# Performance work log

Measured on AMD Instinct MI355X. Metric: run time of the kernel, lower is better.

Reference implementation:

```python
import jax, jax.numpy as jnp
import numpy as np

N = 50000              # total nodes
E = 800000             # random edges (self loops added inside reference, as PyG GATConv does)
FD = 3                 # feature_dim_node
C = 64                 # hidden_channels (= out after heads=1 concat)
OUT = 64               # out_channels of conv2
FC = 512               # fc_hidden_dim
NODES_PER_GRAPH = 5000
NUM_GRAPHS = N // NODES_PER_GRAPH
NEG_SLOPE = 0.2        # PyG GATConv default negative_slope


def _gat(x, W, a_s, a_d, b, src, dst):
    """Single-head PyG GATConv: gather -> leaky_relu -> segment softmax over dst -> scatter-sum."""
    n = x.shape[0]
    h = x @ W                       # [N, C]
    e_s = h @ a_s                   # [N] alpha contribution of source nodes
    e_d = h @ a_d                   # [N] alpha contribution of dest nodes
    e = e_s[src] + e_d[dst]         # [E+N] per-edge logits
    e = jnp.where(e > 0, e, NEG_SLOPE * e)  # leaky_relu
    m = jax.ops.segment_max(e, dst, num_segments=n)
    p = jnp.exp(e - m[dst])
    s = jax.ops.segment_sum(p, dst, num_segments=n)
    alpha = p / s[dst]              # segment softmax over incoming edges of each dst
    out = jax.ops.segment_sum(alpha[:, None] * h[src], dst, num_segments=n)
    return out + b


def setup_inputs() -> dict:
    key = jax.random.key(0)
    ks = jax.random.split(key, 20)
    p = lambda k, shape: (jax.random.normal(k, shape, jnp.float32) * 0.1)
    inp = {
        "x": jax.random.normal(ks[0], (N, FD), jnp.float32),
        "edge_index": jax.random.randint(ks[1], (2, E), 0, N, jnp.int64),
        # conv1: FD -> C
        "W1": p(ks[2], (FD, C)), "as1": p(ks[3], (C,)), "ad1": p(ks[4], (C,)), "b1": p(ks[5], (C,)),
        # 2 hidden convs: C -> C (num_layers - 2 = 2)
        "Wh": p(ks[6], (2, C, C)), "ash": p(ks[7], (2, C)), "adh": p(ks[8], (2, C)), "bh": p(ks[9], (2, C)),
        # conv2: C -> OUT
        "W2": p(ks[10], (C, OUT)), "as2": p(ks[11], (OUT,)), "ad2": p(ks[12], (OUT,)), "b2": p(ks[13], (OUT,)),
        # value head MLP
        "Wv1": p(ks[14], (OUT, FC)), "bv1": p(ks[15], (FC,)),
        "Wv2": p(ks[16], (FC, 1)), "bv2": p(ks[17], (1,)),
    }
    return inp


def reference(x, edge_index, W1, as1, ad1, b1, Wh, ash, adh, bh,
              W2, as2, ad2, b2, Wv1, bv1, Wv2, bv2):
    loops = jnp.arange(N, dtype=edge_index.dtype)
    src = jnp.concatenate([edge_index[0], loops])   # add self loops (PyG default)
    dst = jnp.concatenate([edge_index[1], loops])

    h = jax.nn.relu(_gat(x, W1, as1, ad1, b1, src, dst))
    for i in range(2):  # fixed small layer loop
        h = jax.nn.relu(_gat(h, Wh[i], ash[i], adh[i], bh[i], src, dst))
    h = _gat(h, W2, as2, ad2, b2, src, dst)          # [N, OUT] node embeddings (no relu)

    batch = jnp.arange(N) // NODES_PER_GRAPH          # create_batch_tensor
    pooled = jax.ops.segment_sum(h, batch, num_segments=NUM_GRAPHS) / NODES_PER_GRAPH
    value = jax.nn.relu(pooled @ Wv1 + bv1) @ Wv2 + bv2   # [NUM_GRAPHS, 1]
    return h, pooled, value
```

## Files before the change

### kernel.cpp

```cpp
#include <hip/hip_runtime.h>
#include <hip/hip_fp16.h>
#include <math.h>

#define NN 50000
#define EE 800000
#define TOT_EDGES (EE + NN)
#define FD 3
#define C 64
#define FC 512
#define NODES_PER_GRAPH 5000
#define NUM_GRAPHS 10
#define POOL_CHUNKS 40
#define POOL_NODES_PER_CHUNK 125
#define NEG_SLOPE 0.2f

#define SCAN_BLK 1024
#define SCAN_GRID ((NN + SCAN_BLK - 1) / SCAN_BLK)

#define HC_BLOCKS 1024

#define NPART 8
#define PART_NODES ((NN + NPART - 1) / NPART)
#define CSR_EPT 8
#define CSR_CHUNK (256 * CSR_EPT)
#define CSR_CHUNKS ((TOT_EDGES + CSR_CHUNK - 1) / CSR_CHUNK)


__global__ void k_init_counts(int* counts) {
    int i = blockIdx.x * blockDim.x + threadIdx.x;
    if (i < NN) counts[i] = 0;
}

__global__ void k_count_part(const int* __restrict__ dst, int* __restrict__ counts) {
    int part = blockIdx.x & (NPART - 1);
    int chunk = blockIdx.x >> 3;
    int lo = part * PART_NODES, hi = lo + PART_NODES;
    int base = chunk * CSR_CHUNK + threadIdx.x;
#pragma unroll
    for (int e = 0; e < CSR_EPT; ++e) {
        int i = base + e * 256;
        if (i < TOT_EDGES) {
            int d = (i < EE) ? dst[i] : (i - EE);
            if (d >= lo && d < hi) atomicAdd(&counts[d], 1);
        }
    }
}

__global__ void k_scan1(const int* __restrict__ counts, int* __restrict__ offsets,
                        int* __restrict__ blocksums) {
    int tid = threadIdx.x, blk = blockIdx.x;
    int i = blk * SCAN_BLK + tid;
    int v = (i < NN) ? counts[i] : 0;
    __shared__ int buf[SCAN_BLK];
    buf[tid] = v;
    __syncthreads();
    for (int off = 1; off < SCAN_BLK; off <<= 1) {
        int t = (tid >= off) ? buf[tid - off] : 0;
        __syncthreads();
        buf[tid] += t;
        __syncthreads();
    }
    if (i < NN) offsets[i] = buf[tid] - v;
    if (tid == SCAN_BLK - 1) blocksums[blk] = buf[tid];
}

__global__ void k_scan2(int* __restrict__ blocksums, int* __restrict__ offsets) {
    if (threadIdx.x == 0) {
        int run = 0;
        for (int b = 0; b < SCAN_GRID; ++b) {
            int v = blocksums[b];
            blocksums[b] = run;
            run += v;
        }
        offsets[NN] = run;
    }
}

__global__ void k_scan3(int* __restrict__ offsets, int* __restrict__ cursors,
                        const int* __restrict__ blocksums) {
    int tid = threadIdx.x, blk = blockIdx.x;
    int i = blk * SCAN_BLK + tid;
    if (i < NN) {
        int o = offsets[i] + blocksums[blk];
        offsets[i] = o;
        cursors[i] = o;
    }
}

__global__ void k_scatter_part(const int* __restrict__ src, const int* __restrict__ dst,
                               int* __restrict__ cursors, int* __restrict__ ssrc) {
    int part = blockIdx.x & (NPART - 1);
    int chunk = blockIdx.x >> 3;
    int lo = part * PART_NODES, hi = lo + PART_NODES;
    int base = chunk * CSR_CHUNK + threadIdx.x;
#pragma unroll
    for (int e = 0; e < CSR_EPT; ++e) {
        int i = base + e * 256;
        if (i < TOT_EDGES) {
            int d = (i < EE) ? dst[i] : (i - EE);
            if (d >= lo && d < hi) {
                int s = (i < EE) ? src[i] : d;
                int idx = atomicAdd(&cursors[d], 1);
                ssrc[idx] = s;
            }
        }
    }
}


template<int IN_DIM>
__global__ void k_hcompute_t(const float* __restrict__ x,
                             const float* __restrict__ W,
                             const float* __restrict__ a_s, const float* __restrict__ a_d,
                             __half* __restrict__ h, float* __restrict__ es,
                             float* __restrict__ ed, int nwaves_total) {
    int lane = threadIdx.x & 63;
    int wid = (blockIdx.x * blockDim.x + threadIdx.x) >> 6;

    float wcol[IN_DIM];
#pragma unroll
    for (int k = 0; k < IN_DIM; ++k) wcol[k] = W[k * 64 + lane];
    float asl = a_s[lane], adl = a_d[lane];

    for (int n = wid; n < NN; n += nwaves_total) {
        int nu = __builtin_amdgcn_readfirstlane(n);
        const float* xrow = x + (size_t)nu * IN_DIM;
        float acc = 0.f;
#pragma unroll
        for (int k = 0; k < IN_DIM; ++k) acc = fmaf(xrow[k], wcol[k], acc);
        h[(size_t)nu * 64 + lane] = __float2half(acc);
        float vs = acc * asl;
        float vd = acc * adl;
        for (int w = 32; w >= 1; w >>= 1) {
            vs += __shfl_xor(vs, w);
            vd += __shfl_xor(vd, w);
        }
        if (lane == 0) { es[nu] = vs; ed[nu] = vd; }
    }
}

__global__ void k_aggregate(const __half* __restrict__ h,
                            const float* __restrict__ es, const float* __restrict__ ed,
                            const int* __restrict__ offsets, const int* __restrict__ ssrc,
                            const float* __restrict__ bias,
                            float* __restrict__ out, int do_relu) {
    int gtid = blockIdx.x * blockDim.x + threadIdx.x;
    int n = gtid >> 6;
    int lane = threadIdx.x & 63;
    if (n >= NN) return;
    int beg = offsets[n], end = offsets[n + 1];
    float edn = ed[n];

    int grp = lane >> 3;
    int c   = lane & 7;
    float s = 0.f;
    float acc[8];
#pragma unroll
    for (int i = 0; i < 8; ++i) acc[i] = 0.f;

    for (int j0 = beg; j0 < end; j0 += 8) {
        int jg = j0 + grp;
        if (jg < end) {
            int sj = ssrc[jg];
            float e = es[sj] + edn;
            e = (e > 0.f) ? e : NEG_SLOPE * e;
            float p = __expf(e);
            s += p;
            float4 raw = *(const float4*)&h[(size_t)sj * 64 + c * 8];
            const __half2* hp = (const __half2*)&raw;
#pragma unroll
            for (int q = 0; q < 4; ++q) {
                float2 f = __half22float2(hp[q]);
                acc[2 * q]     = fmaf(p, f.x, acc[2 * q]);
                acc[2 * q + 1] = fmaf(p, f.y, acc[2 * q + 1]);
            }
        }
    }
#pragma unroll
    for (int w = 8; w <= 32; w <<= 1) {
        s += __shfl_xor(s, w);
#pragma unroll
        for (int i = 0; i < 8; ++i) acc[i] += __shfl_xor(acc[i], w);
    }
    if (grp == 0) {
        float inv_s = 1.0f / s;
        float v[8];
#pragma unroll
        for (int i = 0; i < 8; ++i) {
            v[i] = acc[i] * inv_s + bias[c * 8 + i];
            if (do_relu) v[i] = fmaxf(v[i], 0.f);
        }
        *(float4*)&out[(size_t)n * 64 + c * 8]     = make_float4(v[0], v[1], v[2], v[3]);
        *(float4*)&out[(size_t)n * 64 + c * 8 + 4] = make_float4(v[4], v[5], v[6], v[7]);
    }
}


__global__ void k_pool1(const float* __restrict__ h, float* __restrict__ partial) {
    int blk = blockIdx.x;
    int g = blk / POOL_CHUNKS, c = blk % POOL_CHUNKS;
    int wave = threadIdx.x >> 6, lane = threadIdx.x & 63;
    int base = g * NODES_PER_GRAPH + c * POOL_NODES_PER_CHUNK;
    float acc = 0.f;
    for (int i = wave; i < POOL_NODES_PER_CHUNK; i += 4)
        acc += h[(size_t)(base + i) * 64 + lane];
    __shared__ float buf[4][64];
    buf[wave][lane] = acc;
    __syncthreads();
    if (wave == 0)
        partial[blk * 64 + lane] = buf[0][lane] + buf[1][lane] + buf[2][lane] + buf[3][lane];
}

__global__ void k_pool2(const float* __restrict__ partial, float* __restrict__ pooled) {
    int g = blockIdx.x;
    int lane = threadIdx.x;
    float acc = 0.f;
    for (int c = 0; c < POOL_CHUNKS; ++c)
        acc += partial[(g * POOL_CHUNKS + c) * 64 + lane];
    pooled[g * 64 + lane] = acc * (1.0f / NODES_PER_GRAPH);
}

__global__ void k_value(const float* __restrict__ pooled,
                        const float* __restrict__ Wv1, const float* __restrict__ bv1,
                        const float* __restrict__ Wv2, const float* __restrict__ bv2,
                        float* __restrict__ value) {
    int g = blockIdx.x;
    int j = threadIdx.x;
    __shared__ float pl[64];
    if (j < 64) pl[j] = pooled[g * 64 + j];
    __syncthreads();
    float acc = bv1[j];
    for (int c = 0; c < 64; ++c) acc += pl[c] * Wv1[c * 512 + j];
    acc = fmaxf(acc, 0.f);
    float t = acc * Wv2[j];
    for (int w = 32; w >= 1; w >>= 1) t += __shfl_xor(t, w);
    __shared__ float red[8];
    int wave = j >> 6, lane = j & 63;
    if (lane == 0) red[wave] = t;
    __syncthreads();
    if (j == 0) {
        float v = 0.f;
        for (int w = 0; w < 8; ++w) v += red[w];
        value[g] = v + bv2[0];
    }
}


extern "C" void kernel_launch(void* const* d_in, const int* in_sizes, int n_in,
                              void* d_out, int out_size, void* d_ws, size_t ws_size,
                              hipStream_t stream) {
    const float* x   = (const float*)d_in[0];
    const int*   ei  = (const int*)d_in[1];
    const float* W1  = (const float*)d_in[2];
    const float* as1 = (const float*)d_in[3];
    const float* ad1 = (const float*)d_in[4];
    const float* b1  = (const float*)d_in[5];
    const float* Wh  = (const float*)d_in[6];
    const float* ash = (const float*)d_in[7];
    const float* adh = (const float*)d_in[8];
    const float* bh  = (const float*)d_in[9];
    const float* W2  = (const float*)d_in[10];
    const float* as2 = (const float*)d_in[11];
    const float* ad2 = (const float*)d_in[12];
    const float* b2  = (const float*)d_in[13];
    const float* Wv1 = (const float*)d_in[14];
    const float* bv1 = (const float*)d_in[15];
    const float* Wv2 = (const float*)d_in[16];
    const float* bv2 = (const float*)d_in[17];

    const int* e_src = ei;
    const int* e_dst = ei + EE;

    char* p = (char*)d_ws;
    auto carve = [&](size_t bytes) {
        char* r = p;
        p += (bytes + 255) & ~(size_t)255;
        return r;
    };
    int*    counts    = (int*)carve(NN * 4);
    int*    offsets   = (int*)carve((NN + 1) * 4);
    int*    cursors   = (int*)carve(NN * 4);
    int*    ssrc      = (int*)carve(TOT_EDGES * 4);
    int*    blocksums = (int*)carve(SCAN_GRID * 4);
    __half* bufH      = (__half*)carve((size_t)NN * 64 * 2);
    float*  bufB      = (float*)carve((size_t)NN * 64 * 4);
    float*  es        = (float*)carve(NN * 4);
    float*  ed        = (float*)carve(NN * 4);
    float*  partial   = (float*)carve((size_t)NUM_GRAPHS * POOL_CHUNKS * 64 * 4);

    float* out_h      = (float*)d_out;
    float* out_pooled = out_h + (size_t)NN * 64;
    float* out_value  = out_pooled + NUM_GRAPHS * 64;

    k_init_counts<<<(NN + 255) / 256, 256, 0, stream>>>(counts);
    k_count_part<<<NPART * CSR_CHUNKS, 256, 0, stream>>>(e_dst, counts);
    k_scan1<<<SCAN_GRID, SCAN_BLK, 0, stream>>>(counts, offsets, blocksums);
    k_scan2<<<1, 64, 0, stream>>>(blocksums, offsets);
    k_scan3<<<SCAN_GRID, SCAN_BLK, 0, stream>>>(offsets, cursors, blocksums);
    k_scatter_part<<<NPART * CSR_CHUNKS, 256, 0, stream>>>(e_src, e_dst, cursors, ssrc);

    const int HBLK = (NN + 3) / 4;
    const int HC_WAVES = HC_BLOCKS * 256 / 64;

    k_hcompute_t<FD><<<HC_BLOCKS, 256, 0, stream>>>(x, W1, as1, ad1, bufH, es, ed, HC_WAVES);
    k_aggregate<<<HBLK, 256, 0, stream>>>(bufH, es, ed, offsets, ssrc, b1, bufB, 1);

    for (int i = 0; i < 2; ++i) {
        k_hcompute_t<C><<<HC_BLOCKS, 256, 0, stream>>>(bufB, Wh + i * 64 * 64, ash + i * 64,
                                                       adh + i * 64, bufH, es, ed, HC_WAVES);
        k_aggregate<<<HBLK, 256, 0, stream>>>(bufH, es, ed, offsets, ssrc, bh + i * 64, bufB, 1);
    }

    k_hcompute_t<C><<<HC_BLOCKS, 256, 0, stream>>>(bufB, W2, as2, ad2, bufH, es, ed, HC_WAVES);
    k_aggregate<<<HBLK, 256, 0, stream>>>(bufH, es, ed, offsets, ssrc, b2, out_h, 0);

    k_pool1<<<NUM_GRAPHS * POOL_CHUNKS, 256, 0, stream>>>(out_h, partial);
    k_pool2<<<NUM_GRAPHS, 64, 0, stream>>>(partial, out_pooled);
    k_value<<<NUM_GRAPHS, 512, 0, stream>>>(out_pooled, Wv1, bv1, Wv2, bv2, out_value);
}
```

Measured before the change: 290.6 us.

## Fuse next-layer linear transform and attention logits into aggregation kernel

```diff
diff --git a/kernel.cpp b/kernel.cpp
--- a/kernel.cpp
+++ b/kernel.cpp
@@ -18,6 +18,7 @@
 #define SCAN_GRID ((NN + SCAN_BLK - 1) / SCAN_BLK)
 
 #define HC_BLOCKS 1024
+#define AGG_BLOCKS 1024
 
 #define NPART 8
 #define PART_NODES ((NN + NPART - 1) / NPART)
@@ -139,59 +140,95 @@
     }
 }
 
-__global__ void k_aggregate(const __half* __restrict__ h,
+template<int HAS_NEXT>
+__global__ void k_agg_fused(const __half* __restrict__ h,
                             const float* __restrict__ es, const float* __restrict__ ed,
                             const int* __restrict__ offsets, const int* __restrict__ ssrc,
                             const float* __restrict__ bias,
-                            float* __restrict__ out, int do_relu) {
-    int gtid = blockIdx.x * blockDim.x + threadIdx.x;
-    int n = gtid >> 6;
+                            const float* __restrict__ Wn,
+                            const float* __restrict__ asn, const float* __restrict__ adn,
+                            __half* __restrict__ hn, float* __restrict__ esn,
+                            float* __restrict__ edn_out,
+                            float* __restrict__ out_final,
+                            int nwaves_total) {
     int lane = threadIdx.x & 63;
-    if (n >= NN) return;
-    int beg = offsets[n], end = offsets[n + 1];
-    float edn = ed[n];
-
+    int wid = (blockIdx.x * blockDim.x + threadIdx.x) >> 6;
     int grp = lane >> 3;
     int c   = lane & 7;
-    float s = 0.f;
-    float acc[8];
-#pragma unroll
-    for (int i = 0; i < 8; ++i) acc[i] = 0.f;
-
-    for (int j0 = beg; j0 < end; j0 += 8) {
-        int jg = j0 + grp;
-        if (jg < end) {
-            int sj = ssrc[jg];
-            float e = es[sj] + edn;
-            e = (e > 0.f) ? e : NEG_SLOPE * e;
-            float p = __expf(e);
-            s += p;
-            float4 raw = *(const float4*)&h[(size_t)sj * 64 + c * 8];
-            const __half2* hp = (const __half2*)&raw;
-#pragma unroll
-            for (int q = 0; q < 4; ++q) {
-                float2 f = __half22float2(hp[q]);
-                acc[2 * q]     = fmaf(p, f.x, acc[2 * q]);
-                acc[2 * q + 1] = fmaf(p, f.y, acc[2 * q + 1]);
-            }
-        }
-    }
-#pragma unroll
-    for (int w = 8; w <= 32; w <<= 1) {
-        s += __shfl_xor(s, w);
-#pragma unroll
-        for (int i = 0; i < 8; ++i) acc[i] += __shfl_xor(acc[i], w);
-    }
-    if (grp == 0) {
+
+    float wn[HAS_NEXT ? 64 : 1];
+    float asl = 0.f, adl = 0.f;
+    if (HAS_NEXT) {
+#pragma unroll
+        for (int k = 0; k < 64; ++k) wn[k] = Wn[k * 64 + lane];
+        asl = asn[lane];
+        adl = adn[lane];
+    }
+    float4 blo = *(const float4*)&bias[c * 8];
+    float4 bhi = *(const float4*)&bias[c * 8 + 4];
+    float bb[8] = {blo.x, blo.y, blo.z, blo.w, bhi.x, bhi.y, bhi.z, bhi.w};
+
+    for (int n = wid; n < NN; n += nwaves_total) {
+        int beg = offsets[n], end = offsets[n + 1];
+        float ednv = ed[n];
+        float s = 0.f;
+        float acc[8];
+#pragma unroll
+        for (int i = 0; i < 8; ++i) acc[i] = 0.f;
+
+        for (int j0 = beg; j0 < end; j0 += 8) {
+            int jg = j0 + grp;
+            if (jg < end) {
+                int sj = ssrc[jg];
+                float e = es[sj] + ednv;
+                e = (e > 0.f) ? e : NEG_SLOPE * e;
+                float p = __expf(e);
+                s += p;
+                float4 raw = *(const float4*)&h[(size_t)sj * 64 + c * 8];
+                const __half2* hp = (const __half2*)&raw;
+#pragma unroll
+                for (int q = 0; q < 4; ++q) {
+                    float2 f = __half22float2(hp[q]);
+                    acc[2 * q]     = fmaf(p, f.x, acc[2 * q]);
+                    acc[2 * q + 1] = fmaf(p, f.y, acc[2 * q + 1]);
+                }
+            }
+        }
+#pragma unroll
+        for (int w = 8; w <= 32; w <<= 1) {
+            s += __shfl_xor(s, w);
+#pragma unroll
+            for (int i = 0; i < 8; ++i) acc[i] += __shfl_xor(acc[i], w);
+        }
         float inv_s = 1.0f / s;
         float v[8];
 #pragma unroll
         for (int i = 0; i < 8; ++i) {
-            v[i] = acc[i] * inv_s + bias[c * 8 + i];
-            if (do_relu) v[i] = fmaxf(v[i], 0.f);
-        }
-        *(float4*)&out[(size_t)n * 64 + c * 8]     = make_float4(v[0], v[1], v[2], v[3]);
-        *(float4*)&out[(size_t)n * 64 + c * 8 + 4] = make_float4(v[4], v[5], v[6], v[7]);
+            v[i] = acc[i] * inv_s + bb[i];
+            if (HAS_NEXT) v[i] = fmaxf(v[i], 0.f);
+        }
+
+        if (HAS_NEXT) {
+            float hv = 0.f;
+#pragma unroll
+            for (int k = 0; k < 64; ++k) {
+                float rowk = __shfl(v[k & 7], k >> 3);
+                hv = fmaf(rowk, wn[k], hv);
+            }
+            hn[(size_t)n * 64 + lane] = __float2half(hv);
+            float vs = hv * asl;
+            float vd = hv * adl;
+            for (int w = 32; w >= 1; w >>= 1) {
+                vs += __shfl_xor(vs, w);
+                vd += __shfl_xor(vd, w);
+            }
+            if (lane == 0) { esn[n] = vs; edn_out[n] = vd; }
+        } else {
+            if (grp == 0) {
+                *(float4*)&out_final[(size_t)n * 64 + c * 8]     = make_float4(v[0], v[1], v[2], v[3]);
+                *(float4*)&out_final[(size_t)n * 64 + c * 8 + 4] = make_float4(v[4], v[5], v[6], v[7]);
+            }
+        }
     }
 }
 
@@ -282,10 +319,12 @@
     int*    cursors   = (int*)carve(NN * 4);
     int*    ssrc      = (int*)carve(TOT_EDGES * 4);
     int*    blocksums = (int*)carve(SCAN_GRID * 4);
-    __half* bufH      = (__half*)carve((size_t)NN * 64 * 2);
-    float*  bufB      = (float*)carve((size_t)NN * 64 * 4);
-    float*  es        = (float*)carve(NN * 4);
-    float*  ed        = (float*)carve(NN * 4);
+    __half* bufHA     = (__half*)carve((size_t)NN * 64 * 2);
+    __half* bufHB     = (__half*)carve((size_t)NN * 64 * 2);
+    float*  esA       = (float*)carve(NN * 4);
+    float*  edA       = (float*)carve(NN * 4);
+    float*  esB       = (float*)carve(NN * 4);
+    float*  edB       = (float*)carve(NN * 4);
     float*  partial   = (float*)carve((size_t)NUM_GRAPHS * POOL_CHUNKS * 64 * 4);
 
     float* out_h      = (float*)d_out;
@@ -299,20 +338,23 @@
     k_scan3<<<SCAN_GRID, SCAN_BLK, 0, stream>>>(offsets, cursors, blocksums);
     k_scatter_part<<<NPART * CSR_CHUNKS, 256, 0, stream>>>(e_src, e_dst, cursors, ssrc);
 
-    const int HBLK = (NN + 3) / 4;
-    const int HC_WAVES = HC_BLOCKS * 256 / 64;
-
-    k_hcompute_t<FD><<<HC_BLOCKS, 256, 0, stream>>>(x, W1, as1, ad1, bufH, es, ed, HC_WAVES);
-    k_aggregate<<<HBLK, 256, 0, stream>>>(bufH, es, ed, offsets, ssrc, b1, bufB, 1);
-
-    for (int i = 0; i < 2; ++i) {
-        k_hcompute_t<C><<<HC_BLOCKS, 256, 0, stream>>>(bufB, Wh + i * 64 * 64, ash + i * 64,
-                                                       adh + i * 64, bufH, es, ed, HC_WAVES);
-        k_aggregate<<<HBLK, 256, 0, stream>>>(bufH, es, ed, offsets, ssrc, bh + i * 64, bufB, 1);
-    }
-
-    k_hcompute_t<C><<<HC_BLOCKS, 256, 0, stream>>>(bufB, W2, as2, ad2, bufH, es, ed, HC_WAVES);
-    k_aggregate<<<HBLK, 256, 0, stream>>>(bufH, es, ed, offsets, ssrc, b2, out_h, 0);
+    const int HC_WAVES  = HC_BLOCKS * 256 / 64;
+    const int AGG_WAVES = AGG_BLOCKS * 256 / 64;
+
+    k_hcompute_t<FD><<<HC_BLOCKS, 256, 0, stream>>>(x, W1, as1, ad1, bufHA, esA, edA, HC_WAVES);
+
+    k_agg_fused<1><<<AGG_BLOCKS, 256, 0, stream>>>(bufHA, esA, edA, offsets, ssrc, b1,
+                                                   Wh + 0 * 64 * 64, ash + 0 * 64, adh + 0 * 64,
+                                                   bufHB, esB, edB, nullptr, AGG_WAVES);
+    k_agg_fused<1><<<AGG_BLOCKS, 256, 0, stream>>>(bufHB, esB, edB, offsets, ssrc, bh + 0 * 64,
+                                                   Wh + 1 * 64 * 64, ash + 1 * 64, adh + 1 * 64,
+                                                   bufHA, esA, edA, nullptr, AGG_WAVES);
+    k_agg_fused<1><<<AGG_BLOCKS, 256, 0, stream>>>(bufHA, esA, edA, offsets, ssrc, bh + 1 * 64,
+                                                   W2, as2, ad2,
+                                                   bufHB, esB, edB, nullptr, AGG_WAVES);
+    k_agg_fused<0><<<AGG_BLOCKS, 256, 0, stream>>>(bufHB, esB, edB, offsets, ssrc, b2,
+                                                   nullptr, nullptr, nullptr,
+                                                   nullptr, nullptr, nullptr, out_h, AGG_WAVES);
 
     k_pool1<<<NUM_GRAPHS * POOL_CHUNKS, 256, 0, stream>>>(out_h, partial);
     k_pool2<<<NUM_GRAPHS, 64, 0, stream>>>(partial, out_pooled);
```

After: 362.5 us. 1.25x slower.

## Aggregate before transform and fuse next-layer linear and attention logits into aggregation

Applied to the files above, without the earlier changes.

```diff
diff --git a/kernel.cpp b/kernel.cpp
--- a/kernel.cpp
+++ b/kernel.cpp
@@ -17,13 +17,23 @@
 #define SCAN_BLK 1024
 #define SCAN_GRID ((NN + SCAN_BLK - 1) / SCAN_BLK)
 
-#define HC_BLOCKS 1024
+#define AGG_BLOCKS 2048
 
 #define NPART 8
 #define PART_NODES ((NN + NPART - 1) / NPART)
 #define CSR_EPT 8
 #define CSR_CHUNK (256 * CSR_EPT)
 #define CSR_CHUNKS ((TOT_EDGES + CSR_CHUNK - 1) / CSR_CHUNK)
+
+#define OFF_W1AS 0
+#define OFF_W1AD 4
+#define OFF_WAS2 8
+#define OFF_WAD2 72
+#define OFF_WAS3 136
+#define OFF_WAD3 200
+#define OFF_WAS4 264
+#define OFF_WAD4 328
+#define WA_FLOATS 392
 
 
 __global__ void k_init_counts(int* counts) {
@@ -108,90 +118,195 @@
 }
 
 
-template<int IN_DIM>
-__global__ void k_hcompute_t(const float* __restrict__ x,
-                             const float* __restrict__ W,
-                             const float* __restrict__ a_s, const float* __restrict__ a_d,
-                             __half* __restrict__ h, float* __restrict__ es,
-                             float* __restrict__ ed, int nwaves_total) {
-    int lane = threadIdx.x & 63;
-    int wid = (blockIdx.x * blockDim.x + threadIdx.x) >> 6;
-
-    float wcol[IN_DIM];
-#pragma unroll
-    for (int k = 0; k < IN_DIM; ++k) wcol[k] = W[k * 64 + lane];
-    float asl = a_s[lane], adl = a_d[lane];
-
-    for (int n = wid; n < NN; n += nwaves_total) {
-        int nu = __builtin_amdgcn_readfirstlane(n);
-        const float* xrow = x + (size_t)nu * IN_DIM;
-        float acc = 0.f;
-#pragma unroll
-        for (int k = 0; k < IN_DIM; ++k) acc = fmaf(xrow[k], wcol[k], acc);
-        h[(size_t)nu * 64 + lane] = __float2half(acc);
-        float vs = acc * asl;
-        float vd = acc * adl;
-        for (int w = 32; w >= 1; w >>= 1) {
-            vs += __shfl_xor(vs, w);
-            vd += __shfl_xor(vd, w);
-        }
-        if (lane == 0) { es[nu] = vs; ed[nu] = vd; }
-    }
-}
-
-__global__ void k_aggregate(const __half* __restrict__ h,
-                            const float* __restrict__ es, const float* __restrict__ ed,
-                            const int* __restrict__ offsets, const int* __restrict__ ssrc,
-                            const float* __restrict__ bias,
-                            float* __restrict__ out, int do_relu) {
-    int gtid = blockIdx.x * blockDim.x + threadIdx.x;
-    int n = gtid >> 6;
+__global__ void k_prep(const float* __restrict__ W1,
+                       const float* __restrict__ as1, const float* __restrict__ ad1,
+                       const float* __restrict__ Wh,
+                       const float* __restrict__ ash, const float* __restrict__ adh,
+                       const float* __restrict__ W2,
+                       const float* __restrict__ as2, const float* __restrict__ ad2,
+                       float* __restrict__ wa) {
+    int t = threadIdx.x;
+    if (t < FD) {
+        float s = 0.f, d = 0.f;
+        for (int o = 0; o < 64; ++o) {
+            s += W1[t * 64 + o] * as1[o];
+            d += W1[t * 64 + o] * ad1[o];
+        }
+        wa[OFF_W1AS + t] = s;
+        wa[OFF_W1AD + t] = d;
+    }
+    {
+        float s = 0.f, d = 0.f;
+        for (int o = 0; o < 64; ++o) {
+            s += Wh[t * 64 + o] * ash[o];
+            d += Wh[t * 64 + o] * adh[o];
+        }
+        wa[OFF_WAS2 + t] = s;
+        wa[OFF_WAD2 + t] = d;
+    }
+    {
+        float s = 0.f, d = 0.f;
+        for (int o = 0; o < 64; ++o) {
+            s += Wh[4096 + t * 64 + o] * ash[64 + o];
+            d += Wh[4096 + t * 64 + o] * adh[64 + o];
+        }
+        wa[OFF_WAS3 + t] = s;
+        wa[OFF_WAD3 + t] = d;
+    }
+    {
+        float s = 0.f, d = 0.f;
+        for (int o = 0; o < 64; ++o) {
+            s += W2[t * 64 + o] * as2[o];
+            d += W2[t * 64 + o] * ad2[o];
+        }
+        wa[OFF_WAS4 + t] = s;
+        wa[OFF_WAD4 + t] = d;
+    }
+}
+
+
+__global__ void k_attn1(const float* __restrict__ x, const float* __restrict__ wa,
+                        float4* __restrict__ xpad, float* __restrict__ es,
+                        float* __restrict__ ed) {
+    int n = blockIdx.x * blockDim.x + threadIdx.x;
+    if (n >= NN) return;
+    float x0 = x[3 * n], x1 = x[3 * n + 1], x2 = x[3 * n + 2];
+    xpad[n] = make_float4(x0, x1, x2, 0.f);
+    es[n] = x0 * wa[OFF_W1AS] + x1 * wa[OFF_W1AS + 1] + x2 * wa[OFF_W1AS + 2];
+    ed[n] = x0 * wa[OFF_W1AD] + x1 * wa[OFF_W1AD + 1] + x2 * wa[OFF_W1AD + 2];
+}
+
+
+__global__ void k_agg1(const float4* __restrict__ xpad,
+                       const float* __restrict__ es, const float* __restrict__ ed,
+                       const int* __restrict__ offsets, const int* __restrict__ ssrc,
+                       const float* __restrict__ W1, const float* __restrict__ b1,
+                       const float* __restrict__ wa,
+                       __half* __restrict__ xn, float* __restrict__ esn,
+                       float* __restrict__ edn) {
+    int n = (blockIdx.x * blockDim.x + threadIdx.x) >> 6;
     int lane = threadIdx.x & 63;
     if (n >= NN) return;
     int beg = offsets[n], end = offsets[n + 1];
-    float edn = ed[n];
-
+    float ednv = ed[n];
+
+    float s = 0.f, a0 = 0.f, a1 = 0.f, a2 = 0.f;
+    for (int j = beg + lane; j < end; j += 64) {
+        int sj = ssrc[j];
+        float e = es[sj] + ednv;
+        e = (e > 0.f) ? e : NEG_SLOPE * e;
+        float p = __expf(e);
+        float4 xv = xpad[sj];
+        s += p;
+        a0 = fmaf(p, xv.x, a0);
+        a1 = fmaf(p, xv.y, a1);
+        a2 = fmaf(p, xv.z, a2);
+    }
+    for (int w = 32; w >= 1; w >>= 1) {
+        s  += __shfl_xor(s, w);
+        a0 += __shfl_xor(a0, w);
+        a1 += __shfl_xor(a1, w);
+        a2 += __shfl_xor(a2, w);
+    }
+    float inv = 1.0f / s;
+    float y = b1[lane];
+    y = fmaf(a0 * inv, W1[lane], y);
+    y = fmaf(a1 * inv, W1[64 + lane], y);
+    y = fmaf(a2 * inv, W1[128 + lane], y);
+    float xv = fmaxf(y, 0.f);
+    xn[(size_t)n * 64 + lane] = __float2half(xv);
+    float vs = xv * wa[OFF_WAS2 + lane];
+    float vd = xv * wa[OFF_WAD2 + lane];
+    for (int w = 32; w >= 1; w >>= 1) {
+        vs += __shfl_xor(vs, w);
+        vd += __shfl_xor(vd, w);
+    }
+    if (lane == 0) { esn[n] = vs; edn[n] = vd; }
+}
+
+template<int FINAL>
+__launch_bounds__(256, 6)
+__global__ void k_agg_h(const __half* __restrict__ xt,
+                        const float* __restrict__ es, const float* __restrict__ ed,
+                        const int* __restrict__ offsets, const int* __restrict__ ssrc,
+                        const float* __restrict__ Wn, const float* __restrict__ bias,
+                        const float* __restrict__ wasn, const float* __restrict__ wadn,
+                        __half* __restrict__ xn, float* __restrict__ esn,
+                        float* __restrict__ edn_out, float* __restrict__ outF,
+                        int nwaves_total) {
+    int lane = threadIdx.x & 63;
+    int wid = (blockIdx.x * blockDim.x + threadIdx.x) >> 6;
     int grp = lane >> 3;
     int c   = lane & 7;
-    float s = 0.f;
-    float acc[8];
-#pragma unroll
-    for (int i = 0; i < 8; ++i) acc[i] = 0.f;
-
-    for (int j0 = beg; j0 < end; j0 += 8) {
-        int jg = j0 + grp;
-        if (jg < end) {
-            int sj = ssrc[jg];
-            float e = es[sj] + edn;
-            e = (e > 0.f) ? e : NEG_SLOPE * e;
-            float p = __expf(e);
-            s += p;
-            float4 raw = *(const float4*)&h[(size_t)sj * 64 + c * 8];
-            const __half2* hp = (const __half2*)&raw;
-#pragma unroll
-            for (int q = 0; q < 4; ++q) {
-                float2 f = __half22float2(hp[q]);
-                acc[2 * q]     = fmaf(p, f.x, acc[2 * q]);
-                acc[2 * q + 1] = fmaf(p, f.y, acc[2 * q + 1]);
+
+    __half2 wn[32];
+#pragma unroll
+    for (int q = 0; q < 32; ++q)
+        wn[q] = __floats2half2_rn(Wn[(2 * q) * 64 + lane], Wn[(2 * q + 1) * 64 + lane]);
+    float bl = bias[lane];
+    float wsl = FINAL ? 0.f : wasn[lane];
+    float wdl = FINAL ? 0.f : wadn[lane];
+
+    for (int n = wid; n < NN; n += nwaves_total) {
+        int beg = offsets[n], end = offsets[n + 1];
+        float ednv = ed[n];
+        float s = 0.f;
+        float acc[8];
+#pragma unroll
+        for (int i = 0; i < 8; ++i) acc[i] = 0.f;
+
+        for (int j0 = beg; j0 < end; j0 += 8) {
+            int jg = j0 + grp;
+            if (jg < end) {
+                int sj = ssrc[jg];
+                float e = es[sj] + ednv;
+                e = (e > 0.f) ? e : NEG_SLOPE * e;
+                float p = __expf(e);
+                s += p;
+                float4 raw = *(const float4*)&xt[(size_t)sj * 64 + c * 8];
+                const __half2* hp = (const __half2*)&raw;
+#pragma unroll
+                for (int q = 0; q < 4; ++q) {
+                    float2 f = __half22float2(hp[q]);
+                    acc[2 * q]     = fmaf(p, f.x, acc[2 * q]);
+                    acc[2 * q + 1] = fmaf(p, f.y, acc[2 * q + 1]);
+                }
             }
         }
-    }
-#pragma unroll
-    for (int w = 8; w <= 32; w <<= 1) {
-        s += __shfl_xor(s, w);
-#pragma unroll
-        for (int i = 0; i < 8; ++i) acc[i] += __shfl_xor(acc[i], w);
-    }
-    if (grp == 0) {
-        float inv_s = 1.0f / s;
+#pragma unroll
+        for (int w = 8; w <= 32; w <<= 1) {
+            s += __shfl_xor(s, w);
+#pragma unroll
+            for (int i = 0; i < 8; ++i) acc[i] += __shfl_xor(acc[i], w);
+        }
+        float inv = 1.0f / s;
         float v[8];
 #pragma unroll
-        for (int i = 0; i < 8; ++i) {
-            v[i] = acc[i] * inv_s + bias[c * 8 + i];
-            if (do_relu) v[i] = fmaxf(v[i], 0.f);
-        }
-        *(float4*)&out[(size_t)n * 64 + c * 8]     = make_float4(v[0], v[1], v[2], v[3]);
-        *(float4*)&out[(size_t)n * 64 + c * 8 + 4] = make_float4(v[4], v[5], v[6], v[7]);
+        for (int i = 0; i < 8; ++i) v[i] = acc[i] * inv;
+
+        float y = bl;
+#pragma unroll
+        for (int j = 0; j < 32; ++j) {
+            float2 wf = __half22float2(wn[j]);
+            float r0 = __shfl(v[(2 * j) & 7], j >> 2);
+            float r1 = __shfl(v[(2 * j + 1) & 7], j >> 2);
+            y = fmaf(r0, wf.x, y);
+            y = fmaf(r1, wf.y, y);
+        }
+
+        if (FINAL) {
+            outF[(size_t)n * 64 + lane] = y;
+        } else {
+            float xv = fmaxf(y, 0.f);
+            xn[(size_t)n * 64 + lane] = __float2half(xv);
+            float vs = xv * wsl;
+            float vd = xv * wdl;
+            for (int w = 32; w >= 1; w >>= 1) {
+                vs += __shfl_xor(vs, w);
+                vd += __shfl_xor(vd, w);
+            }
+            if (lane == 0) { esn[n] = vs; edn_out[n] = vd; }
+        }
     }
 }
 
@@ -282,10 +397,14 @@
     int*    cursors   = (int*)carve(NN * 4);
     int*    ssrc      = (int*)carve(TOT_EDGES * 4);
     int*    blocksums = (int*)carve(SCAN_GRID * 4);
-    __half* bufH      = (__half*)carve((size_t)NN * 64 * 2);
-    float*  bufB      = (float*)carve((size_t)NN * 64 * 4);
-    float*  es        = (float*)carve(NN * 4);
-    float*  ed        = (float*)carve(NN * 4);
+    float*  wa        = (float*)carve(WA_FLOATS * 4);
+    float4* xpad      = (float4*)carve((size_t)NN * 16);
+    __half* bufA      = (__half*)carve((size_t)NN * 64 * 2);
+    __half* bufB      = (__half*)carve((size_t)NN * 64 * 2);
+    float*  esA       = (float*)carve(NN * 4);
+    float*  edA       = (float*)carve(NN * 4);
+    float*  esB       = (float*)carve(NN * 4);
+    float*  edB       = (float*)carve(NN * 4);
     float*  partial   = (float*)carve((size_t)NUM_GRAPHS * POOL_CHUNKS * 64 * 4);
 
     float* out_h      = (float*)d_out;
@@ -300,19 +419,22 @@
     k_scatter_part<<<NPART * CSR_CHUNKS, 256, 0, stream>>>(e_src, e_dst, cursors, ssrc);
 
     const int HBLK = (NN + 3) / 4;
-    const int HC_WAVES = HC_BLOCKS * 256 / 64;
-
-    k_hcompute_t<FD><<<HC_BLOCKS, 256, 0, stream>>>(x, W1, as1, ad1, bufH, es, ed, HC_WAVES);
-    k_aggregate<<<HBLK, 256, 0, stream>>>(bufH, es, ed, offsets, ssrc, b1, bufB, 1);
-
-    for (int i = 0; i < 2; ++i) {
-        k_hcompute_t<C><<<HC_BLOCKS, 256, 0, stream>>>(bufB, Wh + i * 64 * 64, ash + i * 64,
-                                                       adh + i * 64, bufH, es, ed, HC_WAVES);
-        k_aggregate<<<HBLK, 256, 0, stream>>>(bufH, es, ed, offsets, ssrc, bh + i * 64, bufB, 1);
-    }
-
-    k_hcompute_t<C><<<HC_BLOCKS, 256, 0, stream>>>(bufB, W2, as2, ad2, bufH, es, ed, HC_WAVES);
-    k_aggregate<<<HBLK, 256, 0, stream>>>(bufH, es, ed, offsets, ssrc, b2, out_h, 0);
+    const int AGG_WAVES = AGG_BLOCKS * 256 / 64;
+
+    k_prep<<<1, 64, 0, stream>>>(W1, as1, ad1, Wh, ash, adh, W2, as2, ad2, wa);
+    k_attn1<<<(NN + 255) / 256, 256, 0, stream>>>(x, wa, xpad, esA, edA);
+
+    k_agg1<<<HBLK, 256, 0, stream>>>(xpad, esA, edA, offsets, ssrc, W1, b1, wa,
+                                     bufA, esB, edB);
+    k_agg_h<0><<<AGG_BLOCKS, 256, 0, stream>>>(bufA, esB, edB, offsets, ssrc,
+                                               Wh, bh, wa + OFF_WAS3, wa + OFF_WAD3,
+                                               bufB, esA, edA, nullptr, AGG_WAVES);
+    k_agg_h<0><<<AGG_BLOCKS, 256, 0, stream>>>(bufB, esA, edA, offsets, ssrc,
+                                               Wh + 4096, bh + 64, wa + OFF_WAS4, wa + OFF_WAD4,
+                                               bufA, esB, edB, nullptr, AGG_WAVES);
+    k_agg_h<1><<<AGG_BLOCKS, 256, 0, stream>>>(bufA, esB, edB, offsets, ssrc,
+                                               W2, b2, nullptr, nullptr,
+                                               nullptr, nullptr, nullptr, out_h, AGG_WAVES);
 
     k_pool1<<<NUM_GRAPHS * POOL_CHUNKS, 256, 0, stream>>>(out_h, partial);
     k_pool2<<<NUM_GRAPHS, 64, 0, stream>>>(partial, out_pooled);
```

Measured after the change: 588.2 us. 2.02x slower.
